# Performance work log

Measured on AMD Instinct MI355X. Metric: run time of the kernel, lower is better.

## Reference

```python
import jax, jax.numpy as jnp
import numpy as np

V, E, H = 32000, 512, 512
EH = 2 * H  # encoder output size (bidirectional)
B, T, S = 32, 64, 128


def setup_inputs() -> dict:
    key = jax.random.key(0)
    ks = jax.random.split(key, 16)
    s = 0.02
    return {
        "tgt_inputs": jax.random.randint(ks[0], (B, T), 0, V),
        "hidden": jax.random.normal(ks[1], (2, B, H), jnp.float32),
        "encoder_outputs": jax.random.normal(ks[2], (B, S, EH), jnp.float32),
        "src_mask": jnp.ones((B, S), jnp.bool_),
        "embedding": jax.random.normal(ks[3], (V, E), jnp.float32) * s,
        "Wa": jax.random.normal(ks[4], (EH, H), jnp.float32) * s,  # Linear(H -> 2H), weight [out,in]
        "w_ih0": jax.random.normal(ks[5], (3 * H, E + EH), jnp.float32) * s,
        "w_hh0": jax.random.normal(ks[6], (3 * H, H), jnp.float32) * s,
        "b_ih0": jax.random.normal(ks[7], (3 * H,), jnp.float32) * s,
        "b_hh0": jax.random.normal(ks[8], (3 * H,), jnp.float32) * s,
        "w_ih1": jax.random.normal(ks[9], (3 * H, H), jnp.float32) * s,
        "w_hh1": jax.random.normal(ks[10], (3 * H, H), jnp.float32) * s,
        "b_ih1": jax.random.normal(ks[11], (3 * H,), jnp.float32) * s,
        "b_hh1": jax.random.normal(ks[12], (3 * H,), jnp.float32) * s,
        "fc_w": jax.random.normal(ks[13], (V, H + EH), jnp.float32) * s,
        "fc_b": jax.random.normal(ks[14], (V,), jnp.float32) * s,
    }


def _gru_cell(x, h, w_ih, w_hh, b_ih, b_hh):
    # PyTorch GRU cell math
    gi = x @ w_ih.T + b_ih
    gh = h @ w_hh.T + b_hh
    i_r, i_z, i_n = jnp.split(gi, 3, axis=-1)
    h_r, h_z, h_n = jnp.split(gh, 3, axis=-1)
    r = jax.nn.sigmoid(i_r + h_r)
    z = jax.nn.sigmoid(i_z + h_z)
    n = jnp.tanh(i_n + r * h_n)
    return (1.0 - z) * n + z * h


def reference(tgt_inputs, hidden, encoder_outputs, src_mask, embedding, Wa,
              w_ih0, w_hh0, b_ih0, b_hh0, w_ih1, w_hh1, b_ih1, b_hh1,
              fc_w, fc_b):
    scale = 1.0 / jnp.sqrt(jnp.asarray(EH, encoder_outputs.dtype))

    def step(h, tok):
        emb = embedding[tok]                                   # [B,E]
        q = h[-1] @ Wa.T                                       # [B,2H] general attention
        scores = jnp.einsum('be,bse->bs', q, encoder_outputs) * scale
        scores = jnp.where(src_mask, scores, -jnp.inf)
        attn = jax.nn.softmax(scores, axis=-1)                 # [B,S]
        ctx = jnp.einsum('bs,bse->be', attn, encoder_outputs)  # [B,2H]
        x0 = jnp.concatenate([emb, ctx], axis=-1)              # [B,E+2H]
        h0 = _gru_cell(x0, h[0], w_ih0, w_hh0, b_ih0, b_hh0)
        h1 = _gru_cell(h0, h[1], w_ih1, w_hh1, b_ih1, b_hh1)
        logits = jnp.concatenate([h1, ctx], axis=-1) @ fc_w.T + fc_b  # [B,V]
        return jnp.stack([h0, h1]), logits

    # decode steps consume tokens 0..T-2 (teacher forcing)
    toks = tgt_inputs[:, :-1].T                                # [T-1,B]
    _, logits = jax.lax.scan(step, hidden, toks)
    return jnp.transpose(logits, (1, 0, 2))                    # [B,T-1,V]
```

## Files before the change

### kernel.cpp

```cpp
#include <hip/hip_runtime.h>
#include <cstdint>

typedef __attribute__((ext_vector_type(8))) short bf16x8;
typedef __attribute__((ext_vector_type(4))) float f32x4;

__device__ __forceinline__ float bf2f(unsigned short u) {
  union { unsigned int i; float f; } v;
  v.i = ((unsigned int)u) << 16;
  return v.f;
}
__device__ __forceinline__ unsigned short f2bf(float f) {
  union { float f; unsigned int i; } v;
  v.f = f;
  unsigned int x = v.i;
  return (unsigned short)((x + 0x7FFFu + ((x >> 16) & 1u)) >> 16);
}

__global__ __launch_bounds__(256) void k_init_h(const float* __restrict__ hidden,
                                                float* __restrict__ h0buf,
                                                float* __restrict__ h1buf) {
  int i = blockIdx.x * 256 + threadIdx.x;
  if (i < 16384) h0buf[i] = hidden[i];
  else h1buf[i - 16384] = hidden[i];
}

__global__ __launch_bounds__(256) void k_cvt_enc(const float* __restrict__ enc,
                                                 unsigned short* __restrict__ encb) {
  int i = (blockIdx.x * 256 + threadIdx.x) * 4;
  float4 v = *(const float4*)(enc + i);
  ushort4 o;
  o.x = f2bf(v.x); o.y = f2bf(v.y); o.z = f2bf(v.z); o.w = f2bf(v.w);
  *(ushort4*)(encb + i) = o;
}

__global__ __launch_bounds__(256) void k_encwt(const float* __restrict__ enc,
                                               const float* __restrict__ Wa,
                                               unsigned short* __restrict__ encwt) {
  __shared__ float esh[8 * 1024];
  int tid = threadIdx.x;
  int b = blockIdx.x >> 4;
  int s0 = (blockIdx.x & 15) * 8;
  for (int u = 0; u < 32; u++) {
    int f = u * 256 + tid;
    esh[f] = enc[((size_t)b * 128 + s0 + (f >> 10)) * 1024 + (f & 1023)];
  }
  __syncthreads();
  float acc0[8] = {}, acc1[8] = {};
  for (int e = 0; e < 1024; e++) {
    float w0 = Wa[e * 512 + tid];
    float w1 = Wa[e * 512 + tid + 256];
#pragma unroll
    for (int si = 0; si < 8; si++) {
      float ev = esh[si * 1024 + e];
      acc0[si] += w0 * ev;
      acc1[si] += w1 * ev;
    }
  }
#pragma unroll
  for (int si = 0; si < 8; si++) {
    encwt[((size_t)b * 512 + tid) * 128 + s0 + si] = f2bf(acc0[si]);
    encwt[((size_t)b * 512 + tid + 256) * 128 + s0 + si] = f2bf(acc1[si]);
  }
}

__global__ __launch_bounds__(256) void k_attn(
    const float* __restrict__ h1prev,
    const unsigned short* __restrict__ encwt,
    const unsigned short* __restrict__ encb,
    const int* __restrict__ mask,
    const float* __restrict__ embedding,
    const int* __restrict__ tgt,
    float* __restrict__ x0b,
    unsigned short* __restrict__ states,
    int t) {
  __shared__ float h1sh[512];
  __shared__ float rsh[256];
  __shared__ float ssh[128];
  __shared__ float red2[128];
  int tid = threadIdx.x;
  int b = blockIdx.x;
  h1sh[tid] = h1prev[b * 512 + tid];
  h1sh[tid + 256] = h1prev[b * 512 + tid + 256];
  __syncthreads();
  int s = tid & 127, part = tid >> 7;
  const unsigned short* ew = encwt + ((size_t)b * 512 + part * 256) * 128 + s;
  float pacc = 0.f;
#pragma unroll 4
  for (int h = 0; h < 256; h++)
    pacc += bf2f(ew[h * 128]) * h1sh[part * 256 + h];
  rsh[tid] = pacc;
  __syncthreads();
  if (tid < 128) {
    float sc = (rsh[tid] + rsh[tid + 128]) * 0.03125f;
    if (mask[b * 128 + tid] == 0) sc = -__builtin_huge_valf();
    ssh[tid] = sc;
    red2[tid] = sc;
  }
  __syncthreads();
  for (int st = 64; st > 0; st >>= 1) {
    if (tid < st) red2[tid] = fmaxf(red2[tid], red2[tid + st]);
    __syncthreads();
  }
  float mx = red2[0];
  __syncthreads();
  if (tid < 128) {
    float e = __expf(ssh[tid] - mx);
    ssh[tid] = e;
    red2[tid] = e;
  }
  __syncthreads();
  for (int st = 64; st > 0; st >>= 1) {
    if (tid < st) red2[tid] += red2[tid + st];
    __syncthreads();
  }
  float inv = 1.f / red2[0];
  __syncthreads();
  if (tid < 128) ssh[tid] *= inv;
  __syncthreads();
  int e0 = tid * 4;
  float c0 = 0.f, c1 = 0.f, c2 = 0.f, c3 = 0.f;
  const unsigned short* eb = encb + (size_t)b * 131072 + e0;
  for (int s2 = 0; s2 < 128; s2++) {
    float a = ssh[s2];
    ushort4 ev = *(const ushort4*)(eb + s2 * 1024);
    c0 += a * bf2f(ev.x);
    c1 += a * bf2f(ev.y);
    c2 += a * bf2f(ev.z);
    c3 += a * bf2f(ev.w);
  }
  float4 cv;
  cv.x = c0; cv.y = c1; cv.z = c2; cv.w = c3;
  *(float4*)(x0b + b * 1536 + 512 + e0) = cv;
  ushort4 sv;
  sv.x = f2bf(c0); sv.y = f2bf(c1); sv.z = f2bf(c2); sv.w = f2bf(c3);
  *(ushort4*)(states + (size_t)(t * 32 + b) * 1536 + 512 + e0) = sv;
  int tok = tgt[b * 64 + t];
  x0b[b * 1536 + tid] = embedding[(size_t)tok * 512 + tid];
  x0b[b * 1536 + tid + 256] = embedding[(size_t)tok * 512 + tid + 256];
}

__global__ __launch_bounds__(256) void k_gru(
    const float* __restrict__ x,
    int xK,
    const float* __restrict__ hprev,
    const float* __restrict__ w_ih,
    const float* __restrict__ w_hh,
    const float* __restrict__ b_ih, const float* __restrict__ b_hh,
    float* __restrict__ hout,
    unsigned short* __restrict__ states,
    int srow) {
  __shared__ float xsh[32 * 257];
  __shared__ float red[256 * 4];
  int tid = threadIdx.x;
  int b = tid & 31;
  int jl = (tid >> 5) & 1;
  int kq = tid >> 6;
  int j = blockIdx.x * 2 + jl;
  int kb = kq * 64;
  float gr = 0.f, gz = 0.f, gin = 0.f, ghn = 0.f;
  for (int t0 = 0; t0 < xK; t0 += 256) {
    for (int u = 0; u < 32; u++)
      xsh[u * 257 + tid] = x[u * xK + t0 + tid];
    __syncthreads();
    {
      const float4* w0p = (const float4*)(w_ih + (size_t)j * xK + t0 + kb);
      const float4* w1p = (const float4*)(w_ih + (size_t)(j + 512) * xK + t0 + kb);
      const float4* w2p = (const float4*)(w_ih + (size_t)(j + 1024) * xK + t0 + kb);
      const float* xr = xsh + b * 257 + kb;
#pragma unroll 4
      for (int k4 = 0; k4 < 16; k4++) {
        float4 wa = w0p[k4], wb = w1p[k4], wc = w2p[k4];
        float xv0 = xr[k4 * 4 + 0], xv1 = xr[k4 * 4 + 1];
        float xv2 = xr[k4 * 4 + 2], xv3 = xr[k4 * 4 + 3];
        gr = fmaf(wa.x, xv0, gr); gr = fmaf(wa.y, xv1, gr);
        gr = fmaf(wa.z, xv2, gr); gr = fmaf(wa.w, xv3, gr);
        gz = fmaf(wb.x, xv0, gz); gz = fmaf(wb.y, xv1, gz);
        gz = fmaf(wb.z, xv2, gz); gz = fmaf(wb.w, xv3, gz);
        gin = fmaf(wc.x, xv0, gin); gin = fmaf(wc.y, xv1, gin);
        gin = fmaf(wc.z, xv2, gin); gin = fmaf(wc.w, xv3, gin);
      }
    }
    __syncthreads();
  }
  for (int t0 = 0; t0 < 512; t0 += 256) {
    for (int u = 0; u < 32; u++)
      xsh[u * 257 + tid] = hprev[u * 512 + t0 + tid];
    __syncthreads();
    {
      const float4* w0p = (const float4*)(w_hh + (size_t)j * 512 + t0 + kb);
      const float4* w1p = (const float4*)(w_hh + (size_t)(j + 512) * 512 + t0 + kb);
      const float4* w2p = (const float4*)(w_hh + (size_t)(j + 1024) * 512 + t0 + kb);
      const float* xr = xsh + b * 257 + kb;
#pragma unroll 4
      for (int k4 = 0; k4 < 16; k4++) {
        float4 wa = w0p[k4], wb = w1p[k4], wc = w2p[k4];
        float xv0 = xr[k4 * 4 + 0], xv1 = xr[k4 * 4 + 1];
        float xv2 = xr[k4 * 4 + 2], xv3 = xr[k4 * 4 + 3];
        gr = fmaf(wa.x, xv0, gr); gr = fmaf(wa.y, xv1, gr);
        gr = fmaf(wa.z, xv2, gr); gr = fmaf(wa.w, xv3, gr);
        gz = fmaf(wb.x, xv0, gz); gz = fmaf(wb.y, xv1, gz);
        gz = fmaf(wb.z, xv2, gz); gz = fmaf(wb.w, xv3, gz);
        ghn = fmaf(wc.x, xv0, ghn); ghn = fmaf(wc.y, xv1, ghn);
        ghn = fmaf(wc.z, xv2, ghn); ghn = fmaf(wc.w, xv3, ghn);
      }
    }
    __syncthreads();
  }
  red[tid * 4 + 0] = gr;
  red[tid * 4 + 1] = gz;
  red[tid * 4 + 2] = gin;
  red[tid * 4 + 3] = ghn;
  __syncthreads();
  if (tid < 64) {
#pragma unroll
    for (int g = 1; g < 4; g++) {
      gr += red[(tid + g * 64) * 4 + 0];
      gz += red[(tid + g * 64) * 4 + 1];
      gin += red[(tid + g * 64) * 4 + 2];
      ghn += red[(tid + g * 64) * 4 + 3];
    }
    gr += b_ih[j] + b_hh[j];
    gz += b_ih[j + 512] + b_hh[j + 512];
    gin += b_ih[j + 1024];
    ghn += b_hh[j + 1024];
    float r = 1.f / (1.f + __expf(-gr));
    float zz = 1.f / (1.f + __expf(-gz));
    float nv = gin + r * ghn;
    float e2 = __expf(-2.f * fabsf(nv));
    float th = (1.f - e2) / (1.f + e2);
    th = copysignf(th, nv);
    float hp = hprev[b * 512 + j];
    float hn = (1.f - zz) * th + zz * hp;
    hout[b * 512 + j] = hn;
    if (states) states[(size_t)(srow + b) * 1536 + j] = f2bf(hn);
  }
}

__global__ __launch_bounds__(256) void k_gemm(
    const unsigned short* __restrict__ states,
    const float* __restrict__ fc_w,
    const float* __restrict__ fc_b,
    float* __restrict__ out) {
  __shared__ unsigned short Ash[128 * 40];
  __shared__ unsigned short Bsh[128 * 40];
  int tid = threadIdx.x;
  int bx = blockIdx.x;
  int m0 = (bx & 15) * 128;
  int n0 = (bx >> 4) * 128;
  int lane = tid & 63, wave = tid >> 6;
  int q = lane >> 4, l16 = lane & 15;
  int wrow = (wave >> 1) * 64, wcol = (wave & 1) * 64;
  int arow = tid >> 1, ahalf = tid & 1;
  f32x4 acc[4][4] = {};
  const unsigned short* ag = states + (size_t)(m0 + arow) * 1536 + ahalf * 16;
  const float* bg = fc_w + (size_t)(n0 + arow) * 1536 + ahalf * 16;
  for (int k0 = 0; k0 < 1536; k0 += 32) {
    {
      const int4* src = (const int4*)(ag + k0);
      int4* dst = (int4*)(Ash + arow * 40 + ahalf * 16);
      dst[0] = src[0];
      dst[1] = src[1];
    }
    {
      const float4* src = (const float4*)(bg + k0);
      __align__(16) unsigned short us[16];
#pragma unroll
      for (int i = 0; i < 4; i++) {
        float4 v = src[i];
        us[i * 4 + 0] = f2bf(v.x);
        us[i * 4 + 1] = f2bf(v.y);
        us[i * 4 + 2] = f2bf(v.z);
        us[i * 4 + 3] = f2bf(v.w);
      }
      int4* dst = (int4*)(Bsh + arow * 40 + ahalf * 16);
      dst[0] = ((int4*)us)[0];
      dst[1] = ((int4*)us)[1];
    }
    __syncthreads();
    bf16x8 av[4], bv[4];
#pragma unroll
    for (int i = 0; i < 4; i++) {
      av[i] = *(const bf16x8*)(Ash + (wrow + i * 16 + l16) * 40 + q * 8);
      bv[i] = *(const bf16x8*)(Bsh + (wcol + i * 16 + l16) * 40 + q * 8);
    }
#pragma unroll
    for (int mi = 0; mi < 4; mi++)
#pragma unroll
      for (int ni = 0; ni < 4; ni++)
        acc[mi][ni] = __builtin_amdgcn_mfma_f32_16x16x32_bf16(av[mi], bv[ni], acc[mi][ni], 0, 0, 0);
    __syncthreads();
  }
  float fb[4];
#pragma unroll
  for (int ni = 0; ni < 4; ni++) fb[ni] = fc_b[n0 + wcol + ni * 16 + l16];
#pragma unroll
  for (int mi = 0; mi < 4; mi++) {
#pragma unroll
    for (int r = 0; r < 4; r++) {
      int grow = m0 + wrow + mi * 16 + q * 4 + r;
      if (grow < 2016) {
        int tt = grow >> 5, bb = grow & 31;
        float* op = out + (size_t)bb * 2016000 + (size_t)tt * 32000 + n0 + wcol;
#pragma unroll
        for (int ni = 0; ni < 4; ni++)
          op[ni * 16 + l16] = acc[mi][ni][r] + fb[ni];
      }
    }
  }
}

extern "C" void kernel_launch(void* const* d_in, const int* in_sizes, int n_in,
                              void* d_out, int out_size, void* d_ws, size_t ws_size,
                              hipStream_t stream) {
  const int* tgt = (const int*)d_in[0];
  const float* hidden = (const float*)d_in[1];
  const float* enc = (const float*)d_in[2];
  const int* mask = (const int*)d_in[3];
  const float* embedding = (const float*)d_in[4];
  const float* Wa = (const float*)d_in[5];
  const float* w_ih0 = (const float*)d_in[6];
  const float* w_hh0 = (const float*)d_in[7];
  const float* b_ih0 = (const float*)d_in[8];
  const float* b_hh0 = (const float*)d_in[9];
  const float* w_ih1 = (const float*)d_in[10];
  const float* w_hh1 = (const float*)d_in[11];
  const float* b_ih1 = (const float*)d_in[12];
  const float* b_hh1 = (const float*)d_in[13];
  const float* fc_w = (const float*)d_in[14];
  const float* fc_b = (const float*)d_in[15];
  float* out = (float*)d_out;
  char* ws = (char*)d_ws;

  float* h0buf = (float*)(ws + 0);
  float* h1buf = (float*)(ws + 131072);
  float* x0b = (float*)(ws + 262144);
  unsigned short* encb = (unsigned short*)(ws + 458752);
  unsigned short* encwt = (unsigned short*)(ws + 8847360);
  unsigned short* states = (unsigned short*)(ws + 13041664);

  k_init_h<<<128, 256, 0, stream>>>(hidden, h0buf, h1buf);
  k_cvt_enc<<<4096, 256, 0, stream>>>(enc, encb);
  k_encwt<<<512, 256, 0, stream>>>(enc, Wa, encwt);

  for (int t = 0; t < 63; t++) {
    int rd = t & 1, wr = rd ^ 1;
    k_attn<<<32, 256, 0, stream>>>(h1buf + rd * 16384, encwt, encb, mask,
                                   embedding, tgt, x0b, states, t);
    k_gru<<<256, 256, 0, stream>>>(x0b, 1536, h0buf + rd * 16384, w_ih0, w_hh0,
                                   b_ih0, b_hh0, h0buf + wr * 16384,
                                   (unsigned short*)nullptr, 0);
    k_gru<<<256, 256, 0, stream>>>(h0buf + wr * 16384, 512, h1buf + rd * 16384,
                                   w_ih1, w_hh1, b_ih1, b_hh1, h1buf + wr * 16384,
                                   states, t * 32);
  }

  k_gemm<<<4000, 256, 0, stream>>>(states, fc_w, fc_b, out);
}
```

Before: 5.139 ms.

## Fuse recurrent decode loop into one persistent kernel with grid barriers

Replaces the 189 per-step kernel launches (attention plus two GRU kernels per step) and the three setup kernels with a single persistent 256-block kernel. It synchronises phases with atomic-counter grid barriers and spreads attention across all blocks (8 per batch row). The encwt layout is transposed so score dot products use contiguous bf16x8 loads. The output GEMM block order is swizzled for better cache locality. This removes launch overhead and serialisation at a small attention grid, but relies on all 256 blocks being co-resident and adds spin-barrier cost.

```diff
diff --git a/kernel.cpp b/kernel.cpp
--- a/kernel.cpp
+++ b/kernel.cpp
@@ -16,195 +16,94 @@
   return (unsigned short)((x + 0x7FFFu + ((x >> 16) & 1u)) >> 16);
 }
 
-__global__ __launch_bounds__(256) void k_init_h(const float* __restrict__ hidden,
-                                                float* __restrict__ h0buf,
-                                                float* __restrict__ h1buf) {
-  int i = blockIdx.x * 256 + threadIdx.x;
-  if (i < 16384) h0buf[i] = hidden[i];
-  else h1buf[i - 16384] = hidden[i];
-}
-
-__global__ __launch_bounds__(256) void k_cvt_enc(const float* __restrict__ enc,
-                                                 unsigned short* __restrict__ encb) {
-  int i = (blockIdx.x * 256 + threadIdx.x) * 4;
-  float4 v = *(const float4*)(enc + i);
-  ushort4 o;
-  o.x = f2bf(v.x); o.y = f2bf(v.y); o.z = f2bf(v.z); o.w = f2bf(v.w);
-  *(ushort4*)(encb + i) = o;
-}
-
-__global__ __launch_bounds__(256) void k_encwt(const float* __restrict__ enc,
-                                               const float* __restrict__ Wa,
-                                               unsigned short* __restrict__ encwt) {
-  __shared__ float esh[8 * 1024];
-  int tid = threadIdx.x;
-  int b = blockIdx.x >> 4;
-  int s0 = (blockIdx.x & 15) * 8;
-  for (int u = 0; u < 32; u++) {
-    int f = u * 256 + tid;
-    esh[f] = enc[((size_t)b * 128 + s0 + (f >> 10)) * 1024 + (f & 1023)];
-  }
+struct StepParams {
+  const int* tgt;
+  const int* mask;
+  const float* embedding;
+  const float* enc;
+  const float* Wa;
+  const float* hidden;
+  const float* w_ih0; const float* w_hh0; const float* b_ih0; const float* b_hh0;
+  const float* w_ih1; const float* w_hh1; const float* b_ih1; const float* b_hh1;
+  float* h0buf;
+  float* h1buf;
+  float* x0b;
+  unsigned short* encb;
+  unsigned short* encwt;
+  unsigned short* states;
+  unsigned int* bars;
+};
+
+__device__ __forceinline__ void gbar(unsigned int* c) {
   __syncthreads();
-  float acc0[8] = {}, acc1[8] = {};
-  for (int e = 0; e < 1024; e++) {
-    float w0 = Wa[e * 512 + tid];
-    float w1 = Wa[e * 512 + tid + 256];
-#pragma unroll
-    for (int si = 0; si < 8; si++) {
-      float ev = esh[si * 1024 + e];
-      acc0[si] += w0 * ev;
-      acc1[si] += w1 * ev;
-    }
-  }
-#pragma unroll
-  for (int si = 0; si < 8; si++) {
-    encwt[((size_t)b * 512 + tid) * 128 + s0 + si] = f2bf(acc0[si]);
-    encwt[((size_t)b * 512 + tid + 256) * 128 + s0 + si] = f2bf(acc1[si]);
-  }
-}
-
-__global__ __launch_bounds__(256) void k_attn(
-    const float* __restrict__ h1prev,
-    const unsigned short* __restrict__ encwt,
-    const unsigned short* __restrict__ encb,
-    const int* __restrict__ mask,
-    const float* __restrict__ embedding,
-    const int* __restrict__ tgt,
-    float* __restrict__ x0b,
-    unsigned short* __restrict__ states,
-    int t) {
-  __shared__ float h1sh[512];
-  __shared__ float rsh[256];
-  __shared__ float ssh[128];
-  __shared__ float red2[128];
-  int tid = threadIdx.x;
-  int b = blockIdx.x;
-  h1sh[tid] = h1prev[b * 512 + tid];
-  h1sh[tid + 256] = h1prev[b * 512 + tid + 256];
+  if (threadIdx.x == 0) {
+    __threadfence();
+    __hip_atomic_fetch_add(c, 1u, __ATOMIC_RELAXED, __HIP_MEMORY_SCOPE_AGENT);
+    while (__hip_atomic_load(c, __ATOMIC_RELAXED, __HIP_MEMORY_SCOPE_AGENT) < 256u)
+      __builtin_amdgcn_s_sleep(1);
+    __threadfence();
+  }
   __syncthreads();
-  int s = tid & 127, part = tid >> 7;
-  const unsigned short* ew = encwt + ((size_t)b * 512 + part * 256) * 128 + s;
-  float pacc = 0.f;
-#pragma unroll 4
-  for (int h = 0; h < 256; h++)
-    pacc += bf2f(ew[h * 128]) * h1sh[part * 256 + h];
-  rsh[tid] = pacc;
-  __syncthreads();
-  if (tid < 128) {
-    float sc = (rsh[tid] + rsh[tid + 128]) * 0.03125f;
-    if (mask[b * 128 + tid] == 0) sc = -__builtin_huge_valf();
-    ssh[tid] = sc;
-    red2[tid] = sc;
-  }
-  __syncthreads();
-  for (int st = 64; st > 0; st >>= 1) {
-    if (tid < st) red2[tid] = fmaxf(red2[tid], red2[tid + st]);
-    __syncthreads();
-  }
-  float mx = red2[0];
-  __syncthreads();
-  if (tid < 128) {
-    float e = __expf(ssh[tid] - mx);
-    ssh[tid] = e;
-    red2[tid] = e;
-  }
-  __syncthreads();
-  for (int st = 64; st > 0; st >>= 1) {
-    if (tid < st) red2[tid] += red2[tid + st];
-    __syncthreads();
-  }
-  float inv = 1.f / red2[0];
-  __syncthreads();
-  if (tid < 128) ssh[tid] *= inv;
-  __syncthreads();
-  int e0 = tid * 4;
-  float c0 = 0.f, c1 = 0.f, c2 = 0.f, c3 = 0.f;
-  const unsigned short* eb = encb + (size_t)b * 131072 + e0;
-  for (int s2 = 0; s2 < 128; s2++) {
-    float a = ssh[s2];
-    ushort4 ev = *(const ushort4*)(eb + s2 * 1024);
-    c0 += a * bf2f(ev.x);
-    c1 += a * bf2f(ev.y);
-    c2 += a * bf2f(ev.z);
-    c3 += a * bf2f(ev.w);
-  }
-  float4 cv;
-  cv.x = c0; cv.y = c1; cv.z = c2; cv.w = c3;
-  *(float4*)(x0b + b * 1536 + 512 + e0) = cv;
-  ushort4 sv;
-  sv.x = f2bf(c0); sv.y = f2bf(c1); sv.z = f2bf(c2); sv.w = f2bf(c3);
-  *(ushort4*)(states + (size_t)(t * 32 + b) * 1536 + 512 + e0) = sv;
-  int tok = tgt[b * 64 + t];
-  x0b[b * 1536 + tid] = embedding[(size_t)tok * 512 + tid];
-  x0b[b * 1536 + tid + 256] = embedding[(size_t)tok * 512 + tid + 256];
-}
-
-__global__ __launch_bounds__(256) void k_gru(
-    const float* __restrict__ x,
-    int xK,
+}
+
+__device__ __forceinline__ void gru_phase(
+    const float* __restrict__ x, int xK,
     const float* __restrict__ hprev,
-    const float* __restrict__ w_ih,
-    const float* __restrict__ w_hh,
+    const float* __restrict__ w_ih, const float* __restrict__ w_hh,
     const float* __restrict__ b_ih, const float* __restrict__ b_hh,
-    float* __restrict__ hout,
-    unsigned short* __restrict__ states,
-    int srow) {
-  __shared__ float xsh[32 * 257];
-  __shared__ float red[256 * 4];
-  int tid = threadIdx.x;
+    float* __restrict__ hout, unsigned short* states, int srow,
+    int w, int tid, float* xsh, float* red) {
   int b = tid & 31;
   int jl = (tid >> 5) & 1;
   int kq = tid >> 6;
-  int j = blockIdx.x * 2 + jl;
+  int j = w * 2 + jl;
   int kb = kq * 64;
   float gr = 0.f, gz = 0.f, gin = 0.f, ghn = 0.f;
   for (int t0 = 0; t0 < xK; t0 += 256) {
+    __syncthreads();
+#pragma unroll
     for (int u = 0; u < 32; u++)
       xsh[u * 257 + tid] = x[u * xK + t0 + tid];
     __syncthreads();
-    {
-      const float4* w0p = (const float4*)(w_ih + (size_t)j * xK + t0 + kb);
-      const float4* w1p = (const float4*)(w_ih + (size_t)(j + 512) * xK + t0 + kb);
-      const float4* w2p = (const float4*)(w_ih + (size_t)(j + 1024) * xK + t0 + kb);
-      const float* xr = xsh + b * 257 + kb;
+    const float4* w0p = (const float4*)(w_ih + (size_t)j * xK + t0 + kb);
+    const float4* w1p = (const float4*)(w_ih + (size_t)(j + 512) * xK + t0 + kb);
+    const float4* w2p = (const float4*)(w_ih + (size_t)(j + 1024) * xK + t0 + kb);
+    const float* xr = xsh + b * 257 + kb;
 #pragma unroll 4
-      for (int k4 = 0; k4 < 16; k4++) {
-        float4 wa = w0p[k4], wb = w1p[k4], wc = w2p[k4];
-        float xv0 = xr[k4 * 4 + 0], xv1 = xr[k4 * 4 + 1];
-        float xv2 = xr[k4 * 4 + 2], xv3 = xr[k4 * 4 + 3];
-        gr = fmaf(wa.x, xv0, gr); gr = fmaf(wa.y, xv1, gr);
-        gr = fmaf(wa.z, xv2, gr); gr = fmaf(wa.w, xv3, gr);
-        gz = fmaf(wb.x, xv0, gz); gz = fmaf(wb.y, xv1, gz);
-        gz = fmaf(wb.z, xv2, gz); gz = fmaf(wb.w, xv3, gz);
-        gin = fmaf(wc.x, xv0, gin); gin = fmaf(wc.y, xv1, gin);
-        gin = fmaf(wc.z, xv2, gin); gin = fmaf(wc.w, xv3, gin);
-      }
-    }
-    __syncthreads();
+    for (int k4 = 0; k4 < 16; k4++) {
+      float4 wa = w0p[k4], wb = w1p[k4], wc = w2p[k4];
+      float xv0 = xr[k4 * 4 + 0], xv1 = xr[k4 * 4 + 1];
+      float xv2 = xr[k4 * 4 + 2], xv3 = xr[k4 * 4 + 3];
+      gr = fmaf(wa.x, xv0, gr); gr = fmaf(wa.y, xv1, gr);
+      gr = fmaf(wa.z, xv2, gr); gr = fmaf(wa.w, xv3, gr);
+      gz = fmaf(wb.x, xv0, gz); gz = fmaf(wb.y, xv1, gz);
+      gz = fmaf(wb.z, xv2, gz); gz = fmaf(wb.w, xv3, gz);
+      gin = fmaf(wc.x, xv0, gin); gin = fmaf(wc.y, xv1, gin);
+      gin = fmaf(wc.z, xv2, gin); gin = fmaf(wc.w, xv3, gin);
+    }
   }
   for (int t0 = 0; t0 < 512; t0 += 256) {
+    __syncthreads();
+#pragma unroll
     for (int u = 0; u < 32; u++)
       xsh[u * 257 + tid] = hprev[u * 512 + t0 + tid];
     __syncthreads();
-    {
-      const float4* w0p = (const float4*)(w_hh + (size_t)j * 512 + t0 + kb);
-      const float4* w1p = (const float4*)(w_hh + (size_t)(j + 512) * 512 + t0 + kb);
-      const float4* w2p = (const float4*)(w_hh + (size_t)(j + 1024) * 512 + t0 + kb);
-      const float* xr = xsh + b * 257 + kb;
+    const float4* w0p = (const float4*)(w_hh + (size_t)j * 512 + t0 + kb);
+    const float4* w1p = (const float4*)(w_hh + (size_t)(j + 512) * 512 + t0 + kb);
+    const float4* w2p = (const float4*)(w_hh + (size_t)(j + 1024) * 512 + t0 + kb);
+    const float* xr = xsh + b * 257 + kb;
 #pragma unroll 4
-      for (int k4 = 0; k4 < 16; k4++) {
-        float4 wa = w0p[k4], wb = w1p[k4], wc = w2p[k4];
-        float xv0 = xr[k4 * 4 + 0], xv1 = xr[k4 * 4 + 1];
-        float xv2 = xr[k4 * 4 + 2], xv3 = xr[k4 * 4 + 3];
-        gr = fmaf(wa.x, xv0, gr); gr = fmaf(wa.y, xv1, gr);
-        gr = fmaf(wa.z, xv2, gr); gr = fmaf(wa.w, xv3, gr);
-        gz = fmaf(wb.x, xv0, gz); gz = fmaf(wb.y, xv1, gz);
-        gz = fmaf(wb.z, xv2, gz); gz = fmaf(wb.w, xv3, gz);
-        ghn = fmaf(wc.x, xv0, ghn); ghn = fmaf(wc.y, xv1, ghn);
-        ghn = fmaf(wc.z, xv2, ghn); ghn = fmaf(wc.w, xv3, ghn);
-      }
-    }
-    __syncthreads();
+    for (int k4 = 0; k4 < 16; k4++) {
+      float4 wa = w0p[k4], wb = w1p[k4], wc = w2p[k4];
+      float xv0 = xr[k4 * 4 + 0], xv1 = xr[k4 * 4 + 1];
+      float xv2 = xr[k4 * 4 + 2], xv3 = xr[k4 * 4 + 3];
+      gr = fmaf(wa.x, xv0, gr); gr = fmaf(wa.y, xv1, gr);
+      gr = fmaf(wa.z, xv2, gr); gr = fmaf(wa.w, xv3, gr);
+      gz = fmaf(wb.x, xv0, gz); gz = fmaf(wb.y, xv1, gz);
+      gz = fmaf(wb.z, xv2, gz); gz = fmaf(wb.w, xv3, gz);
+      ghn = fmaf(wc.x, xv0, ghn); ghn = fmaf(wc.y, xv1, ghn);
+      ghn = fmaf(wc.z, xv2, ghn); ghn = fmaf(wc.w, xv3, ghn);
+    }
   }
   red[tid * 4 + 0] = gr;
   red[tid * 4 + 1] = gz;
@@ -236,6 +135,137 @@
   }
 }
 
+__global__ __launch_bounds__(256, 1) void k_steps(StepParams p) {
+  __shared__ float xsh[32 * 257];
+  __shared__ float red[1024];
+  __shared__ float h1sh[512];
+  __shared__ float ssh[128];
+  __shared__ float red2[128];
+  int tid = threadIdx.x;
+  int w = blockIdx.x;
+
+  {
+    int idx = w * 256 + tid;
+    if (idx < 16384) p.h0buf[idx] = p.hidden[idx];
+    else if (idx < 32768) p.h1buf[idx - 16384] = p.hidden[idx];
+    for (int r = 0; r < 16; r++) {
+      size_t i4 = (size_t)r * 65536 + idx;
+      float4 v = *(const float4*)(p.enc + i4 * 4);
+      ushort4 o;
+      o.x = f2bf(v.x); o.y = f2bf(v.y); o.z = f2bf(v.z); o.w = f2bf(v.w);
+      *(ushort4*)(p.encb + i4 * 4) = o;
+    }
+    for (int blk = w; blk < 512; blk += 256) {
+      int b = blk >> 4, s0 = (blk & 15) * 8;
+      __syncthreads();
+      for (int u = 0; u < 32; u++) {
+        int f = u * 256 + tid;
+        xsh[f] = p.enc[((size_t)b * 128 + s0 + (f >> 10)) * 1024 + (f & 1023)];
+      }
+      __syncthreads();
+      float acc0[8] = {}, acc1[8] = {};
+      for (int e = 0; e < 1024; e++) {
+        float w0 = p.Wa[e * 512 + tid];
+        float w1 = p.Wa[e * 512 + tid + 256];
+#pragma unroll
+        for (int si = 0; si < 8; si++) {
+          float ev = xsh[si * 1024 + e];
+          acc0[si] += w0 * ev;
+          acc1[si] += w1 * ev;
+        }
+      }
+#pragma unroll
+      for (int si = 0; si < 8; si++) {
+        p.encwt[((size_t)b * 128 + s0 + si) * 512 + tid] = f2bf(acc0[si]);
+        p.encwt[((size_t)b * 128 + s0 + si) * 512 + tid + 256] = f2bf(acc1[si]);
+      }
+    }
+  }
+  unsigned int* bar = p.bars;
+  gbar(bar++);
+
+  int ab = w >> 3, ec = w & 7;
+  for (int t = 0; t < 63; t++) {
+    int rd = t & 1, wr = rd ^ 1;
+    const float* h1prev = p.h1buf + rd * 16384;
+    h1sh[tid] = h1prev[ab * 512 + tid];
+    h1sh[tid + 256] = h1prev[ab * 512 + tid + 256];
+    __syncthreads();
+    {
+      int s = tid & 127, part = tid >> 7;
+      const unsigned short* ew = p.encwt + ((size_t)ab * 128 + s) * 512 + part * 256;
+      const float* hh = h1sh + part * 256;
+      float pacc = 0.f;
+#pragma unroll 8
+      for (int hc = 0; hc < 32; hc++) {
+        bf16x8 v = *(const bf16x8*)(ew + hc * 8);
+        const float* h8 = hh + hc * 8;
+        pacc += bf2f((unsigned short)v[0]) * h8[0] + bf2f((unsigned short)v[1]) * h8[1]
+              + bf2f((unsigned short)v[2]) * h8[2] + bf2f((unsigned short)v[3]) * h8[3]
+              + bf2f((unsigned short)v[4]) * h8[4] + bf2f((unsigned short)v[5]) * h8[5]
+              + bf2f((unsigned short)v[6]) * h8[6] + bf2f((unsigned short)v[7]) * h8[7];
+      }
+      red[tid] = pacc;
+    }
+    __syncthreads();
+    if (tid < 128) {
+      float sc = (red[tid] + red[tid + 128]) * 0.03125f;
+      if (p.mask[ab * 128 + tid] == 0) sc = -__builtin_huge_valf();
+      ssh[tid] = sc;
+      red2[tid] = sc;
+    }
+    __syncthreads();
+    for (int st = 64; st > 0; st >>= 1) {
+      if (tid < st) red2[tid] = fmaxf(red2[tid], red2[tid + st]);
+      __syncthreads();
+    }
+    float mx = red2[0];
+    __syncthreads();
+    if (tid < 128) {
+      float e = __expf(ssh[tid] - mx);
+      ssh[tid] = e;
+      red2[tid] = e;
+    }
+    __syncthreads();
+    for (int st = 64; st > 0; st >>= 1) {
+      if (tid < st) red2[tid] += red2[tid + st];
+      __syncthreads();
+    }
+    float inv = 1.f / red2[0];
+    __syncthreads();
+    if (tid < 128) ssh[tid] *= inv;
+    __syncthreads();
+    {
+      int el = tid & 127, sh_ = tid >> 7;
+      const unsigned short* eb = p.encb + (size_t)ab * 131072 + ec * 128 + el;
+      int sbase = sh_ * 64;
+      float c = 0.f;
+#pragma unroll 8
+      for (int s2 = 0; s2 < 64; s2++)
+        c += ssh[sbase + s2] * bf2f(eb[(size_t)(sbase + s2) * 1024]);
+      red[tid] = c;
+    }
+    __syncthreads();
+    if (tid < 128) {
+      float cv = red[tid] + red[tid + 128];
+      p.x0b[ab * 1536 + 512 + ec * 128 + tid] = cv;
+      p.states[(size_t)(t * 32 + ab) * 1536 + 512 + ec * 128 + tid] = f2bf(cv);
+    }
+    {
+      int tok = p.tgt[ab * 64 + t];
+      if (tid < 64)
+        p.x0b[ab * 1536 + ec * 64 + tid] = p.embedding[(size_t)tok * 512 + ec * 64 + tid];
+    }
+    gbar(bar++);
+    gru_phase(p.x0b, 1536, p.h0buf + rd * 16384, p.w_ih0, p.w_hh0, p.b_ih0, p.b_hh0,
+              p.h0buf + wr * 16384, (unsigned short*)nullptr, 0, w, tid, xsh, red);
+    gbar(bar++);
+    gru_phase(p.h0buf + wr * 16384, 512, p.h1buf + rd * 16384, p.w_ih1, p.w_hh1,
+              p.b_ih1, p.b_hh1, p.h1buf + wr * 16384, p.states, t * 32, w, tid, xsh, red);
+    gbar(bar++);
+  }
+}
+
 __global__ __launch_bounds__(256) void k_gemm(
     const unsigned short* __restrict__ states,
     const float* __restrict__ fc_w,
@@ -245,8 +275,9 @@
   __shared__ unsigned short Bsh[128 * 40];
   int tid = threadIdx.x;
   int bx = blockIdx.x;
-  int m0 = (bx & 15) * 128;
-  int n0 = (bx >> 4) * 128;
+  int bid = (bx & 7) * 500 + (bx >> 3);
+  int m0 = (bid & 15) * 128;
+  int n0 = (bid >> 4) * 128;
   int lane = tid & 63, wave = tid >> 6;
   int q = lane >> 4, l16 = lane & 15;
   int wrow = (wave >> 1) * 64, wcol = (wave & 1) * 64;
@@ -337,22 +368,19 @@
   unsigned short* encb = (unsigned short*)(ws + 458752);
   unsigned short* encwt = (unsigned short*)(ws + 8847360);
   unsigned short* states = (unsigned short*)(ws + 13041664);
-
-  k_init_h<<<128, 256, 0, stream>>>(hidden, h0buf, h1buf);
-  k_cvt_enc<<<4096, 256, 0, stream>>>(enc, encb);
-  k_encwt<<<512, 256, 0, stream>>>(enc, Wa, encwt);
-
-  for (int t = 0; t < 63; t++) {
-    int rd = t & 1, wr = rd ^ 1;
-    k_attn<<<32, 256, 0, stream>>>(h1buf + rd * 16384, encwt, encb, mask,
-                                   embedding, tgt, x0b, states, t);
-    k_gru<<<256, 256, 0, stream>>>(x0b, 1536, h0buf + rd * 16384, w_ih0, w_hh0,
-                                   b_ih0, b_hh0, h0buf + wr * 16384,
-                                   (unsigned short*)nullptr, 0);
-    k_gru<<<256, 256, 0, stream>>>(h0buf + wr * 16384, 512, h1buf + rd * 16384,
-                                   w_ih1, w_hh1, b_ih1, b_hh1, h1buf + wr * 16384,
-                                   states, t * 32);
-  }
+  unsigned int* bars = (unsigned int*)(ws + 19234816);
+
+  hipMemsetAsync(bars, 0, 4096, stream);
+
+  StepParams p;
+  p.tgt = tgt; p.mask = mask; p.embedding = embedding; p.enc = enc; p.Wa = Wa;
+  p.hidden = hidden;
+  p.w_ih0 = w_ih0; p.w_hh0 = w_hh0; p.b_ih0 = b_ih0; p.b_hh0 = b_hh0;
+  p.w_ih1 = w_ih1; p.w_hh1 = w_hh1; p.b_ih1 = b_ih1; p.b_hh1 = b_hh1;
+  p.h0buf = h0buf; p.h1buf = h1buf; p.x0b = x0b;
+  p.encb = encb; p.encwt = encwt; p.states = states; p.bars = bars;
+
+  k_steps<<<dim3(256), dim3(256), 0, stream>>>(p);
 
   k_gemm<<<4000, 256, 0, stream>>>(states, fc_w, fc_b, out);
 }
```

After: 10.76 ms. +109.3%, slower.
